# Performance work log

Measured on AMD Instinct MI355X. Metric: run time of the kernel, lower is better.

The kernel has to match this reference:

```python
import jax, jax.numpy as jnp
import numpy as np

BS, NCH, H, NAGGR, R = 8192, 4, 256, 4, 8  # batch, max_output_degree, h_size, n_aggr, rank


def _xavier(k, shape):
    fan_in = int(np.prod(shape[:-1]))
    fan_out = int(shape[-1])
    s = float(np.sqrt(6.0 / (fan_in + fan_out)))
    return jax.random.uniform(k, shape, jnp.float32, -s, s)


def setup_inputs() -> dict:
    key = jax.random.key(0)
    ks = jax.random.split(key, 6)
    return {
        "neighbour_h": jax.random.normal(ks[0], (BS, NCH, H), jnp.float32),
        "U": _xavier(ks[1], (NCH, NAGGR, H, R)),
        "b": _xavier(ks[2], (NCH, NAGGR, 1, R)),
        "U_out": _xavier(ks[3], (NAGGR, R, H)),
        "b_out": _xavier(ks[4], (NAGGR, 1, H)),
        "T": _xavier(ks[5], (NAGGR,) + (R + 1,) * NCH + (R,)),
    }


def reference(neighbour_h, U, b, U_out, b_out, T):
    bs = neighbour_h.shape[0]
    # per-child projection: matmul([bs,nch,1,1,h], [nch,naggr,h,r]) + b, squeezed -> [bs,nch,naggr,r]
    x = jnp.einsum('bch,cahr->bcar', neighbour_h, U) + b[:, :, 0, :]
    ones = jnp.ones((bs, NAGGR, 1), x.dtype)
    # AugmentedTensor chained contraction (vectorized over the n_aggr loop):
    # first mode: [bs,naggr,r+1] @ [naggr,r+1,(r+1)^(nch-1)*r]
    h0 = jnp.concatenate([x[:, 0], ones], axis=-1)          # [bs,naggr,r+1]
    ris = jnp.einsum('baq,aqx->bax', h0, T.reshape(NAGGR, R + 1, -1))
    for i in range(1, NCH):  # contract remaining modes one by one
        hi = jnp.concatenate([x[:, i], ones], axis=-1)      # [bs,naggr,r+1]
        ris = ris.reshape(bs, NAGGR, R + 1, -1)
        ris = jnp.einsum('baq,baqx->bax', hi, ris)
    # ris: [bs,naggr,r]; output projection + bias -> [bs,naggr,h] -> [bs,naggr*h]
    out = jnp.einsum('bar,arh->bah', ris, U_out) + b_out[:, 0, :]
    return out.reshape(bs, -1)
```

## Files before the change

### kernel.cpp

```cpp
#include <hip/hip_runtime.h>

#define TT_ISTRIDE 672
#define TT_ELEMS (4 * 81 * 672)
#define CHUNK_FLOATS (9 * 672)
#define CHUNK_F4 (CHUNK_FLOATS / 4)

__global__ void t_transpose(const float* __restrict__ T, float* __restrict__ Tt) {
    int idx = blockIdx.x * 256 + threadIdx.x;
    if (idx >= TT_ELEMS) return;
    int col  = idx % 84;
    int t1   = idx / 84;
    int r    = t1 & 7;
    int rest = t1 / 8;
    int jt   = col / 28;
    int kk   = col - jt * 28;
    Tt[idx] = (kk < 27) ? T[rest * 648 + (jt * 27 + kk) * 8 + r] : 0.0f;
}

#define GLL(gsrc, ldst) __builtin_amdgcn_global_load_lds( \
    (const __attribute__((address_space(1))) void*)(gsrc), \
    (__attribute__((address_space(3))) void*)(ldst), 16, 0, 0)

__global__ __launch_bounds__(512, 4) void hosvd_fused(
    const float* __restrict__ nh,
    const float* __restrict__ U,
    const float* __restrict__ bi,
    const float* __restrict__ Uo,
    const float* __restrict__ bo,
    const float* __restrict__ Tt,
    float* __restrict__ out) {
    __shared__ union {
        float u[4 * 256 * 8];
        float tc[2][CHUNK_FLOATS];
    } sm;
    __shared__ float uo_lds[8 * 256];
    __shared__ float h_t[36][64];
    __shared__ float ris_s[64][8];

    const int t    = threadIdx.x;
    const int lane = t & 63;
    const int widr = t >> 6;
    const int wg   = (blockIdx.x & 7) * 64 + (blockIdx.x >> 3);
    const int a    = wg & 3;
    const int b0   = (wg >> 2) << 6;

    for (int idx = t; idx < 8192; idx += 512) {
        int c   = idx >> 11;
        int rem = idx & 2047;
        sm.u[idx] = U[((c * 4 + a) << 11) + rem];
    }
    for (int idx = t; idx < 2048; idx += 512)
        uo_lds[idx] = Uo[(a << 11) + idx];
    __syncthreads();

    {
        const int c  = widr >> 1;
        const int r0 = (widr & 1) << 2;
        const float* nhp   = nh + (size_t)(b0 + lane) * 1024 + (size_t)c * 256;
        const float* ubase = sm.u + (c << 11) + r0;
        float4 acc = make_float4(0.f, 0.f, 0.f, 0.f);
        #pragma unroll 4
        for (int h = 0; h < 256; h += 4) {
            float4 v  = *(const float4*)(nhp + h);
            float4 u0 = *(const float4*)(ubase + ((h + 0) << 3));
            float4 u1 = *(const float4*)(ubase + ((h + 1) << 3));
            float4 u2 = *(const float4*)(ubase + ((h + 2) << 3));
            float4 u3 = *(const float4*)(ubase + ((h + 3) << 3));
            acc.x = fmaf(v.x, u0.x, acc.x); acc.y = fmaf(v.x, u0.y, acc.y);
            acc.z = fmaf(v.x, u0.z, acc.z); acc.w = fmaf(v.x, u0.w, acc.w);
            acc.x = fmaf(v.y, u1.x, acc.x); acc.y = fmaf(v.y, u1.y, acc.y);
            acc.z = fmaf(v.y, u1.z, acc.z); acc.w = fmaf(v.y, u1.w, acc.w);
            acc.x = fmaf(v.z, u2.x, acc.x); acc.y = fmaf(v.z, u2.y, acc.y);
            acc.z = fmaf(v.z, u2.z, acc.z); acc.w = fmaf(v.z, u2.w, acc.w);
            acc.x = fmaf(v.w, u3.x, acc.x); acc.y = fmaf(v.w, u3.y, acc.y);
            acc.z = fmaf(v.w, u3.z, acc.z); acc.w = fmaf(v.w, u3.w, acc.w);
        }
        const float4 bb4 = *(const float4*)&bi[((c * 4 + a) << 3) + r0];
        h_t[c * 9 + r0 + 0][lane] = acc.x + bb4.x;
        h_t[c * 9 + r0 + 1][lane] = acc.y + bb4.y;
        h_t[c * 9 + r0 + 2][lane] = acc.z + bb4.z;
        h_t[c * 9 + r0 + 3][lane] = acc.w + bb4.w;
        if (r0) h_t[c * 9 + 8][lane] = 1.0f;
    }
    __syncthreads();

    {
        float h0v[9], h1v[9], h2v[9], h3v[9];
        #pragma unroll
        for (int q = 0; q < 9; ++q) {
            h0v[q] = h_t[q][lane];
            h1v[q] = h_t[9 + q][lane];
            h2v[q] = h_t[18 + q][lane];
            h3v[q] = h_t[27 + q][lane];
        }
        const float* Tw = Tt + (size_t)(a * 81) * TT_ISTRIDE;
        float A = 0.0f;

        {
            const float* s = Tw;
            float* d = sm.tc[0];
            GLL(s + 4 * t, d + 4 * t);
            GLL(s + 4 * (512 + t), d + 4 * (512 + t));
            if (t < CHUNK_F4 - 1024) GLL(s + 4 * (1024 + t), d + 4 * (1024 + t));
        }

        #pragma unroll 1
        for (int c = 0; c < 9; ++c) {
            if (c < 8) {
                const float* s = Tw + (size_t)(c + 1) * CHUNK_FLOATS;
                float* d = sm.tc[(c + 1) & 1];
                GLL(s + 4 * t, d + 4 * t);
                GLL(s + 4 * (512 + t), d + 4 * (512 + t));
                if (t < CHUNK_F4 - 1024) GLL(s + 4 * (1024 + t), d + 4 * (1024 + t));
                asm volatile("s_waitcnt vmcnt(3)" ::: "memory");
            } else {
                asm volatile("s_waitcnt vmcnt(0)" ::: "memory");
            }
            __builtin_amdgcn_s_barrier();
            asm volatile("" ::: "memory");

            const float* tcp = sm.tc[c & 1] + widr * 84;
            const float h0c  = h0v[c];
            #pragma unroll 1
            for (int q1 = 0; q1 < 9; ++q1) {
                const float* tp = tcp + q1 * TT_ISTRIDE;
                float dd = 0.0f;
                #pragma unroll
                for (int jt = 0; jt < 3; ++jt) {
                    float s[28];
                    #pragma unroll
                    for (int m = 0; m < 7; ++m)
                        *(float4*)(s + 4 * m) = *(const float4*)(tp + jt * 28 + 4 * m);
                    float e0 = 0.f, e1 = 0.f, e2 = 0.f;
                    #pragma unroll
                    for (int m = 0; m < 9; ++m) {
                        e0 = fmaf(s[m],      h3v[m], e0);
                        e1 = fmaf(s[9 + m],  h3v[m], e1);
                        e2 = fmaf(s[18 + m], h3v[m], e2);
                    }
                    dd += fmaf(h2v[3 * jt + 2], e2,
                           fmaf(h2v[3 * jt + 1], e1, h2v[3 * jt] * e0));
                }
                A = fmaf(h0c * h1v[q1], dd, A);
            }
            asm volatile("" ::: "memory");
            __builtin_amdgcn_s_barrier();
        }
        ris_s[lane][widr] = A;
    }
    __syncthreads();

    {
        const int h  = t & 255;
        const int bh = t >> 8;
        const float bov = bo[(a << 8) + h];
        const float u0 = uo_lds[h],            u1 = uo_lds[256 + h];
        const float u2 = uo_lds[512 + h],      u3 = uo_lds[768 + h];
        const float u4 = uo_lds[1024 + h],     u5 = uo_lds[1280 + h];
        const float u6 = uo_lds[1536 + h],     u7 = uo_lds[1792 + h];
        float* op = out + (size_t)(b0 + (bh << 5)) * 1024 + (a << 8) + h;
        #pragma unroll 4
        for (int bb = 0; bb < 32; ++bb) {
            const int bidx = (bh << 5) + bb;
            const float4 rlo = *(const float4*)&ris_s[bidx][0];
            const float4 rhi = *(const float4*)&ris_s[bidx][4];
            float v = bov;
            v = fmaf(rlo.x, u0, v); v = fmaf(rlo.y, u1, v);
            v = fmaf(rlo.z, u2, v); v = fmaf(rlo.w, u3, v);
            v = fmaf(rhi.x, u4, v); v = fmaf(rhi.y, u5, v);
            v = fmaf(rhi.z, u6, v); v = fmaf(rhi.w, u7, v);
            op[(size_t)bb * 1024] = v;
        }
    }
}

extern "C" void kernel_launch(void* const* d_in, const int* in_sizes, int n_in,
                              void* d_out, int out_size, void* d_ws, size_t ws_size,
                              hipStream_t stream) {
    (void)in_sizes; (void)n_in; (void)out_size; (void)ws_size;
    const float* nh = (const float*)d_in[0];
    const float* U  = (const float*)d_in[1];
    const float* bi = (const float*)d_in[2];
    const float* Uo = (const float*)d_in[3];
    const float* bo = (const float*)d_in[4];
    const float* T  = (const float*)d_in[5];
    float* outp = (float*)d_out;
    float* Tt   = (float*)d_ws;

    t_transpose<<<(TT_ELEMS + 255) / 256, 256, 0, stream>>>(T, Tt);
    hosvd_fused<<<512, 512, 0, stream>>>(nh, U, bi, Uo, bo, Tt, outp);
}
```

Measured before the change: 100.3 us.

## Process two 64-row batch tiles per workgroup to reuse staged T chunks

Each workgroup now handles 128 batch rows instead of 64, with each thread computing two rows (A and B) in the projection and tensor contraction. Every T chunk loaded into LDS is reused for twice as many rows, so global-to-LDS traffic and barriers per row are halved. The grid drops to 256 blocks and launch bounds relax to 2 blocks per CU. This raises register pressure and lowers parallelism and occupancy, which on a large-CU GPU may leave some CUs idle.

```diff
diff --git a/kernel.cpp b/kernel.cpp
--- a/kernel.cpp
+++ b/kernel.cpp
@@ -21,7 +21,7 @@
     (const __attribute__((address_space(1))) void*)(gsrc), \
     (__attribute__((address_space(3))) void*)(ldst), 16, 0, 0)
 
-__global__ __launch_bounds__(512, 4) void hosvd_fused(
+__global__ __launch_bounds__(512, 2) void hosvd_fused(
     const float* __restrict__ nh,
     const float* __restrict__ U,
     const float* __restrict__ bi,
@@ -34,15 +34,15 @@
         float tc[2][CHUNK_FLOATS];
     } sm;
     __shared__ float uo_lds[8 * 256];
-    __shared__ float h_t[36][64];
-    __shared__ float ris_s[64][8];
+    __shared__ float h_t[36][128];
+    __shared__ float ris_s[128][8];
 
     const int t    = threadIdx.x;
     const int lane = t & 63;
     const int widr = t >> 6;
-    const int wg   = (blockIdx.x & 7) * 64 + (blockIdx.x >> 3);
+    const int wg   = (blockIdx.x & 7) * 32 + (blockIdx.x >> 3);
     const int a    = wg & 3;
-    const int b0   = (wg >> 2) << 6;
+    const int b0   = (wg >> 2) << 7;
 
     for (int idx = t; idx < 8192; idx += 512) {
         int c   = idx >> 11;
@@ -56,45 +56,64 @@
     {
         const int c  = widr >> 1;
         const int r0 = (widr & 1) << 2;
-        const float* nhp   = nh + (size_t)(b0 + lane) * 1024 + (size_t)c * 256;
+        const float* nhA   = nh + (size_t)(b0 + lane) * 1024 + (size_t)c * 256;
+        const float* nhB   = nhA + 64 * 1024;
         const float* ubase = sm.u + (c << 11) + r0;
-        float4 acc = make_float4(0.f, 0.f, 0.f, 0.f);
+        float4 accA = make_float4(0.f, 0.f, 0.f, 0.f);
+        float4 accB = make_float4(0.f, 0.f, 0.f, 0.f);
         #pragma unroll 4
         for (int h = 0; h < 256; h += 4) {
-            float4 v  = *(const float4*)(nhp + h);
+            float4 vA = *(const float4*)(nhA + h);
+            float4 vB = *(const float4*)(nhB + h);
             float4 u0 = *(const float4*)(ubase + ((h + 0) << 3));
             float4 u1 = *(const float4*)(ubase + ((h + 1) << 3));
             float4 u2 = *(const float4*)(ubase + ((h + 2) << 3));
             float4 u3 = *(const float4*)(ubase + ((h + 3) << 3));
-            acc.x = fmaf(v.x, u0.x, acc.x); acc.y = fmaf(v.x, u0.y, acc.y);
-            acc.z = fmaf(v.x, u0.z, acc.z); acc.w = fmaf(v.x, u0.w, acc.w);
-            acc.x = fmaf(v.y, u1.x, acc.x); acc.y = fmaf(v.y, u1.y, acc.y);
-            acc.z = fmaf(v.y, u1.z, acc.z); acc.w = fmaf(v.y, u1.w, acc.w);
-            acc.x = fmaf(v.z, u2.x, acc.x); acc.y = fmaf(v.z, u2.y, acc.y);
-            acc.z = fmaf(v.z, u2.z, acc.z); acc.w = fmaf(v.z, u2.w, acc.w);
-            acc.x = fmaf(v.w, u3.x, acc.x); acc.y = fmaf(v.w, u3.y, acc.y);
-            acc.z = fmaf(v.w, u3.z, acc.z); acc.w = fmaf(v.w, u3.w, acc.w);
+            accA.x = fmaf(vA.x, u0.x, accA.x); accA.y = fmaf(vA.x, u0.y, accA.y);
+            accA.z = fmaf(vA.x, u0.z, accA.z); accA.w = fmaf(vA.x, u0.w, accA.w);
+            accA.x = fmaf(vA.y, u1.x, accA.x); accA.y = fmaf(vA.y, u1.y, accA.y);
+            accA.z = fmaf(vA.y, u1.z, accA.z); accA.w = fmaf(vA.y, u1.w, accA.w);
+            accA.x = fmaf(vA.z, u2.x, accA.x); accA.y = fmaf(vA.z, u2.y, accA.y);
+            accA.z = fmaf(vA.z, u2.z, accA.z); accA.w = fmaf(vA.z, u2.w, accA.w);
+            accA.x = fmaf(vA.w, u3.x, accA.x); accA.y = fmaf(vA.w, u3.y, accA.y);
+            accA.z = fmaf(vA.w, u3.z, accA.z); accA.w = fmaf(vA.w, u3.w, accA.w);
+            accB.x = fmaf(vB.x, u0.x, accB.x); accB.y = fmaf(vB.x, u0.y, accB.y);
+            accB.z = fmaf(vB.x, u0.z, accB.z); accB.w = fmaf(vB.x, u0.w, accB.w);
+            accB.x = fmaf(vB.y, u1.x, accB.x); accB.y = fmaf(vB.y, u1.y, accB.y);
+            accB.z = fmaf(vB.y, u1.z, accB.z); accB.w = fmaf(vB.y, u1.w, accB.w);
+            accB.x = fmaf(vB.z, u2.x, accB.x); accB.y = fmaf(vB.z, u2.y, accB.y);
+            accB.z = fmaf(vB.z, u2.z, accB.z); accB.w = fmaf(vB.z, u2.w, accB.w);
+            accB.x = fmaf(vB.w, u3.x, accB.x); accB.y = fmaf(vB.w, u3.y, accB.y);
+            accB.z = fmaf(vB.w, u3.z, accB.z); accB.w = fmaf(vB.w, u3.w, accB.w);
         }
         const float4 bb4 = *(const float4*)&bi[((c * 4 + a) << 3) + r0];
-        h_t[c * 9 + r0 + 0][lane] = acc.x + bb4.x;
-        h_t[c * 9 + r0 + 1][lane] = acc.y + bb4.y;
-        h_t[c * 9 + r0 + 2][lane] = acc.z + bb4.z;
-        h_t[c * 9 + r0 + 3][lane] = acc.w + bb4.w;
-        if (r0) h_t[c * 9 + 8][lane] = 1.0f;
+        h_t[c * 9 + r0 + 0][lane]      = accA.x + bb4.x;
+        h_t[c * 9 + r0 + 1][lane]      = accA.y + bb4.y;
+        h_t[c * 9 + r0 + 2][lane]      = accA.z + bb4.z;
+        h_t[c * 9 + r0 + 3][lane]      = accA.w + bb4.w;
+        h_t[c * 9 + r0 + 0][lane + 64] = accB.x + bb4.x;
+        h_t[c * 9 + r0 + 1][lane + 64] = accB.y + bb4.y;
+        h_t[c * 9 + r0 + 2][lane + 64] = accB.z + bb4.z;
+        h_t[c * 9 + r0 + 3][lane + 64] = accB.w + bb4.w;
+        if (r0) {
+            h_t[c * 9 + 8][lane]      = 1.0f;
+            h_t[c * 9 + 8][lane + 64] = 1.0f;
+        }
     }
     __syncthreads();
 
     {
-        float h0v[9], h1v[9], h2v[9], h3v[9];
+        float h0A[9], h1A[9], h2A[9], h3A[9];
+        float h0B[9], h1B[9], h2B[9], h3B[9];
         #pragma unroll
         for (int q = 0; q < 9; ++q) {
-            h0v[q] = h_t[q][lane];
-            h1v[q] = h_t[9 + q][lane];
-            h2v[q] = h_t[18 + q][lane];
-            h3v[q] = h_t[27 + q][lane];
+            h0A[q] = h_t[q][lane];      h0B[q] = h_t[q][lane + 64];
+            h1A[q] = h_t[9 + q][lane];  h1B[q] = h_t[9 + q][lane + 64];
+            h2A[q] = h_t[18 + q][lane]; h2B[q] = h_t[18 + q][lane + 64];
+            h3A[q] = h_t[27 + q][lane]; h3B[q] = h_t[27 + q][lane + 64];
         }
         const float* Tw = Tt + (size_t)(a * 81) * TT_ISTRIDE;
-        float A = 0.0f;
+        float AA = 0.0f, AB = 0.0f;
 
         {
             const float* s = Tw;
@@ -120,33 +139,41 @@
             asm volatile("" ::: "memory");
 
             const float* tcp = sm.tc[c & 1] + widr * 84;
-            const float h0c  = h0v[c];
-            #pragma unroll 1
+            const float h0cA = h0A[c], h0cB = h0B[c];
+            #pragma unroll 3
             for (int q1 = 0; q1 < 9; ++q1) {
                 const float* tp = tcp + q1 * TT_ISTRIDE;
-                float dd = 0.0f;
+                float ddA = 0.0f, ddB = 0.0f;
                 #pragma unroll
                 for (int jt = 0; jt < 3; ++jt) {
                     float s[28];
                     #pragma unroll
                     for (int m = 0; m < 7; ++m)
                         *(float4*)(s + 4 * m) = *(const float4*)(tp + jt * 28 + 4 * m);
-                    float e0 = 0.f, e1 = 0.f, e2 = 0.f;
+                    float e0A = 0.f, e1A = 0.f, e2A = 0.f;
+                    float e0B = 0.f, e1B = 0.f, e2B = 0.f;
                     #pragma unroll
                     for (int m = 0; m < 9; ++m) {
-                        e0 = fmaf(s[m],      h3v[m], e0);
-                        e1 = fmaf(s[9 + m],  h3v[m], e1);
-                        e2 = fmaf(s[18 + m], h3v[m], e2);
+                        e0A = fmaf(s[m],      h3A[m], e0A);
+                        e1A = fmaf(s[9 + m],  h3A[m], e1A);
+                        e2A = fmaf(s[18 + m], h3A[m], e2A);
+                        e0B = fmaf(s[m],      h3B[m], e0B);
+                        e1B = fmaf(s[9 + m],  h3B[m], e1B);
+                        e2B = fmaf(s[18 + m], h3B[m], e2B);
                     }
-                    dd += fmaf(h2v[3 * jt + 2], e2,
-                           fmaf(h2v[3 * jt + 1], e1, h2v[3 * jt] * e0));
+                    ddA = fmaf(h2A[3 * jt], e0A, fmaf(h2A[3 * jt + 1], e1A,
+                          fmaf(h2A[3 * jt + 2], e2A, ddA)));
+                    ddB = fmaf(h2B[3 * jt], e0B, fmaf(h2B[3 * jt + 1], e1B,
+                          fmaf(h2B[3 * jt + 2], e2B, ddB)));
                 }
-                A = fmaf(h0c * h1v[q1], dd, A);
+                AA = fmaf(h0cA * h1A[q1], ddA, AA);
+                AB = fmaf(h0cB * h1B[q1], ddB, AB);
             }
             asm volatile("" ::: "memory");
             __builtin_amdgcn_s_barrier();
         }
-        ris_s[lane][widr] = A;
+        ris_s[lane][widr]      = AA;
+        ris_s[lane + 64][widr] = AB;
     }
     __syncthreads();
 
@@ -158,10 +185,10 @@
         const float u2 = uo_lds[512 + h],      u3 = uo_lds[768 + h];
         const float u4 = uo_lds[1024 + h],     u5 = uo_lds[1280 + h];
         const float u6 = uo_lds[1536 + h],     u7 = uo_lds[1792 + h];
-        float* op = out + (size_t)(b0 + (bh << 5)) * 1024 + (a << 8) + h;
+        float* op = out + (size_t)(b0 + (bh << 6)) * 1024 + (a << 8) + h;
         #pragma unroll 4
-        for (int bb = 0; bb < 32; ++bb) {
-            const int bidx = (bh << 5) + bb;
+        for (int bb = 0; bb < 64; ++bb) {
+            const int bidx = (bh << 6) + bb;
             const float4 rlo = *(const float4*)&ris_s[bidx][0];
             const float4 rhi = *(const float4*)&ris_s[bidx][4];
             float v = bov;
@@ -188,5 +215,5 @@
     float* Tt   = (float*)d_ws;
 
     t_transpose<<<(TT_ELEMS + 255) / 256, 256, 0, stream>>>(T, Tt);
-    hosvd_fused<<<512, 512, 0, stream>>>(nh, U, bi, Uo, bo, Tt, outp);
+    hosvd_fused<<<256, 512, 0, stream>>>(nh, U, bi, Uo, bo, Tt, outp);
 }
```

Measured after the change: 96.55 us. 1.04x faster.

## Split fused kernel into projection, chain-contraction and output kernels with 4x batch reuse

Applied to the files above, without the earlier changes.

Replaces the single fused kernel with three kernels. The first computes the per-child projections into a workspace. The second streams the core tensor through LDS for 256 batch rows per block, giving each thread four batch rows so every tensor chunk load is reused four times, and splits the first-mode index across two halves for parallelism. The third sums the two partial results and applies the output projection with vectorized stores. This cuts how often the core tensor is re-read from LDS and global memory, at the cost of extra launches, workspace round-trips and higher register pressure.

```diff
diff --git a/kernel.cpp b/kernel.cpp
--- a/kernel.cpp
+++ b/kernel.cpp
@@ -2,8 +2,9 @@
 
 #define TT_ISTRIDE 672
 #define TT_ELEMS (4 * 81 * 672)
-#define CHUNK_FLOATS (9 * 672)
-#define CHUNK_F4 (CHUNK_FLOATS / 4)
+#define WS_H   217728
+#define WS_RIS 1397376
+#define RIS_IHALF_STRIDE 262144
 
 __global__ void t_transpose(const float* __restrict__ T, float* __restrict__ Tt) {
     int idx = blockIdx.x * 256 + threadIdx.x;
@@ -21,156 +22,207 @@
     (const __attribute__((address_space(1))) void*)(gsrc), \
     (__attribute__((address_space(3))) void*)(ldst), 16, 0, 0)
 
-__global__ __launch_bounds__(512, 4) void hosvd_fused(
-    const float* __restrict__ nh,
-    const float* __restrict__ U,
-    const float* __restrict__ bi,
-    const float* __restrict__ Uo,
-    const float* __restrict__ bo,
-    const float* __restrict__ Tt,
-    float* __restrict__ out) {
-    __shared__ union {
-        float u[4 * 256 * 8];
-        float tc[2][CHUNK_FLOATS];
-    } sm;
-    __shared__ float uo_lds[8 * 256];
-    __shared__ float h_t[36][64];
-    __shared__ float ris_s[64][8];
+#define KEEP(x) asm volatile("" : "+v"(x))
+
+__global__ __launch_bounds__(512, 4) void k1_phasex(
+    const float* __restrict__ nh, const float* __restrict__ U,
+    const float* __restrict__ bi, float* __restrict__ h_ws) {
+    __shared__ float nh_s[128 * 68];
+    __shared__ float u_s[8 * 68];
+    const int t  = threadIdx.x;
+    const int a  = blockIdx.x >> 6;
+    const int b0 = (blockIdx.x & 63) << 7;
+    const int b  = t & 127;
+    const int rp = t >> 7;
+
+    #pragma unroll 1
+    for (int c = 0; c < 4; ++c) {
+        float acc0 = 0.f, acc1 = 0.f;
+        #pragma unroll 1
+        for (int hq = 0; hq < 4; ++hq) {
+            __syncthreads();
+            #pragma unroll
+            for (int k = 0; k < 4; ++k) {
+                int idx = t + (k << 9);
+                int row = idx >> 4, col = (idx & 15) << 2;
+                *(float4*)(nh_s + row * 68 + col) =
+                    *(const float4*)(nh + (size_t)(b0 + row) * 1024 + (c << 8) + (hq << 6) + col);
+            }
+            u_s[(t & 7) * 68 + (t >> 3)] =
+                U[(((c << 2) + a) << 11) + (((hq << 6) + (t >> 3)) << 3) + (t & 7)];
+            __syncthreads();
+            const float* nhp = nh_s + b * 68;
+            const float* u0p = u_s + rp * 68;
+            const float* u1p = u_s + (rp + 4) * 68;
+            #pragma unroll
+            for (int hh = 0; hh < 64; hh += 4) {
+                float4 v  = *(const float4*)(nhp + hh);
+                float4 ua = *(const float4*)(u0p + hh);
+                float4 ub = *(const float4*)(u1p + hh);
+                acc0 = fmaf(v.x, ua.x, acc0); acc0 = fmaf(v.y, ua.y, acc0);
+                acc0 = fmaf(v.z, ua.z, acc0); acc0 = fmaf(v.w, ua.w, acc0);
+                acc1 = fmaf(v.x, ub.x, acc1); acc1 = fmaf(v.y, ub.y, acc1);
+                acc1 = fmaf(v.z, ub.z, acc1); acc1 = fmaf(v.w, ub.w, acc1);
+            }
+        }
+        acc0 += bi[(((c << 2) + a) << 3) + rp];
+        acc1 += bi[(((c << 2) + a) << 3) + rp + 4];
+        size_t hb = ((size_t)a * 8192 + b0 + b) * 36 + c * 9;
+        h_ws[hb + rp]     = acc0;
+        h_ws[hb + rp + 4] = acc1;
+        if (rp == 0) h_ws[hb + 8] = 1.0f;
+    }
+}
+
+__global__ __launch_bounds__(512, 2) void k2_chain(
+    const float* __restrict__ Tt, const float* __restrict__ h_ws,
+    float* __restrict__ risP) {
+    __shared__ float tc[2][9 * 672];
+    __shared__ float h_s[36 * 260];
 
     const int t    = threadIdx.x;
     const int lane = t & 63;
     const int widr = t >> 6;
-    const int wg   = (blockIdx.x & 7) * 64 + (blockIdx.x >> 3);
-    const int a    = wg & 3;
-    const int b0   = (wg >> 2) << 6;
-
-    for (int idx = t; idx < 8192; idx += 512) {
-        int c   = idx >> 11;
-        int rem = idx & 2047;
-        sm.u[idx] = U[((c * 4 + a) << 11) + rem];
-    }
-    for (int idx = t; idx < 2048; idx += 512)
-        uo_lds[idx] = Uo[(a << 11) + idx];
+    const int ihalf = blockIdx.x >> 7;
+    const int a     = (blockIdx.x >> 5) & 3;
+    const int b0    = (blockIdx.x & 31) << 8;
+    const int q0base = ihalf ? 4 : 0;
+    const int NC     = ihalf ? 5 : 4;
+
+    const float* Tw = Tt + (size_t)a * 54432 + (size_t)q0base * 6048;
+
+    {
+        const float* s = Tw;
+        float* d = tc[0];
+        GLL(s + 4 * t, d + 4 * t);
+        GLL(s + 4 * (512 + t), d + 4 * (512 + t));
+        if (t < 488) GLL(s + 4 * (1024 + t), d + 4 * (1024 + t));
+    }
+    for (int idx = t; idx < 2304; idx += 512) {
+        int bb = idx / 9, j = idx % 9;
+        float4 v = *(const float4*)(h_ws + ((size_t)a * 8192 + b0 + bb) * 36 + j * 4);
+        h_s[(4 * j + 0) * 260 + bb] = v.x;
+        h_s[(4 * j + 1) * 260 + bb] = v.y;
+        h_s[(4 * j + 2) * 260 + bb] = v.z;
+        h_s[(4 * j + 3) * 260 + bb] = v.w;
+    }
     __syncthreads();
 
-    {
-        const int c  = widr >> 1;
-        const int r0 = (widr & 1) << 2;
-        const float* nhp   = nh + (size_t)(b0 + lane) * 1024 + (size_t)c * 256;
-        const float* ubase = sm.u + (c << 11) + r0;
-        float4 acc = make_float4(0.f, 0.f, 0.f, 0.f);
-        #pragma unroll 4
-        for (int h = 0; h < 256; h += 4) {
-            float4 v  = *(const float4*)(nhp + h);
-            float4 u0 = *(const float4*)(ubase + ((h + 0) << 3));
-            float4 u1 = *(const float4*)(ubase + ((h + 1) << 3));
-            float4 u2 = *(const float4*)(ubase + ((h + 2) << 3));
-            float4 u3 = *(const float4*)(ubase + ((h + 3) << 3));
-            acc.x = fmaf(v.x, u0.x, acc.x); acc.y = fmaf(v.x, u0.y, acc.y);
-            acc.z = fmaf(v.x, u0.z, acc.z); acc.w = fmaf(v.x, u0.w, acc.w);
-            acc.x = fmaf(v.y, u1.x, acc.x); acc.y = fmaf(v.y, u1.y, acc.y);
-            acc.z = fmaf(v.y, u1.z, acc.z); acc.w = fmaf(v.y, u1.w, acc.w);
-            acc.x = fmaf(v.z, u2.x, acc.x); acc.y = fmaf(v.z, u2.y, acc.y);
-            acc.z = fmaf(v.z, u2.z, acc.z); acc.w = fmaf(v.z, u2.w, acc.w);
-            acc.x = fmaf(v.w, u3.x, acc.x); acc.y = fmaf(v.w, u3.y, acc.y);
-            acc.z = fmaf(v.w, u3.z, acc.z); acc.w = fmaf(v.w, u3.w, acc.w);
-        }
-        const float4 bb4 = *(const float4*)&bi[((c * 4 + a) << 3) + r0];
-        h_t[c * 9 + r0 + 0][lane] = acc.x + bb4.x;
-        h_t[c * 9 + r0 + 1][lane] = acc.y + bb4.y;
-        h_t[c * 9 + r0 + 2][lane] = acc.z + bb4.z;
-        h_t[c * 9 + r0 + 3][lane] = acc.w + bb4.w;
-        if (r0) h_t[c * 9 + 8][lane] = 1.0f;
-    }
-    __syncthreads();
-
-    {
-        float h0v[9], h1v[9], h2v[9], h3v[9];
+    float h2v[4][9], h3v[4][9];
+    #pragma unroll
+    for (int k = 0; k < 4; ++k) {
         #pragma unroll
         for (int q = 0; q < 9; ++q) {
-            h0v[q] = h_t[q][lane];
-            h1v[q] = h_t[9 + q][lane];
-            h2v[q] = h_t[18 + q][lane];
-            h3v[q] = h_t[27 + q][lane];
-        }
-        const float* Tw = Tt + (size_t)(a * 81) * TT_ISTRIDE;
-        float A = 0.0f;
-
-        {
-            const float* s = Tw;
-            float* d = sm.tc[0];
+            h2v[k][q] = h_s[(18 + q) * 260 + lane + 64 * k];
+            h3v[k][q] = h_s[(27 + q) * 260 + lane + 64 * k];
+        }
+    }
+    #pragma unroll
+    for (int k = 0; k < 4; ++k) {
+        #pragma unroll
+        for (int q = 0; q < 9; ++q) { KEEP(h2v[k][q]); KEEP(h3v[k][q]); }
+    }
+
+    float A0 = 0.f, A1 = 0.f, A2 = 0.f, A3 = 0.f;
+
+    #pragma unroll 1
+    for (int c = 0; c < NC; ++c) {
+        if (c < NC - 1) {
+            const float* s = Tw + (size_t)(c + 1) * 6048;
+            float* d = tc[(c + 1) & 1];
             GLL(s + 4 * t, d + 4 * t);
             GLL(s + 4 * (512 + t), d + 4 * (512 + t));
-            if (t < CHUNK_F4 - 1024) GLL(s + 4 * (1024 + t), d + 4 * (1024 + t));
-        }
+            if (t < 488) GLL(s + 4 * (1024 + t), d + 4 * (1024 + t));
+            asm volatile("s_waitcnt vmcnt(3)" ::: "memory");
+        } else {
+            asm volatile("s_waitcnt vmcnt(0)" ::: "memory");
+        }
+        __builtin_amdgcn_s_barrier();
+        asm volatile("" ::: "memory");
+
+        const float* tb = tc[c & 1] + widr * 84;
+        float h0c[4];
+        #pragma unroll
+        for (int k = 0; k < 4; ++k)
+            h0c[k] = h_s[(q0base + c) * 260 + lane + 64 * k];
 
         #pragma unroll 1
-        for (int c = 0; c < 9; ++c) {
-            if (c < 8) {
-                const float* s = Tw + (size_t)(c + 1) * CHUNK_FLOATS;
-                float* d = sm.tc[(c + 1) & 1];
-                GLL(s + 4 * t, d + 4 * t);
-                GLL(s + 4 * (512 + t), d + 4 * (512 + t));
-                if (t < CHUNK_F4 - 1024) GLL(s + 4 * (1024 + t), d + 4 * (1024 + t));
-                asm volatile("s_waitcnt vmcnt(3)" ::: "memory");
-            } else {
-                asm volatile("s_waitcnt vmcnt(0)" ::: "memory");
-            }
-            __builtin_amdgcn_s_barrier();
-            asm volatile("" ::: "memory");
-
-            const float* tcp = sm.tc[c & 1] + widr * 84;
-            const float h0c  = h0v[c];
-            #pragma unroll 1
-            for (int q1 = 0; q1 < 9; ++q1) {
-                const float* tp = tcp + q1 * TT_ISTRIDE;
-                float dd = 0.0f;
+        for (int q1 = 0; q1 < 9; ++q1) {
+            float h1q[4];
+            #pragma unroll
+            for (int k = 0; k < 4; ++k)
+                h1q[k] = h_s[(9 + q1) * 260 + lane + 64 * k];
+            const float* tp = tb + q1 * TT_ISTRIDE;
+            float dd[4] = {0.f, 0.f, 0.f, 0.f};
+            #pragma unroll
+            for (int jt = 0; jt < 3; ++jt) {
+                float s[28];
                 #pragma unroll
-                for (int jt = 0; jt < 3; ++jt) {
-                    float s[28];
-                    #pragma unroll
-                    for (int m = 0; m < 7; ++m)
-                        *(float4*)(s + 4 * m) = *(const float4*)(tp + jt * 28 + 4 * m);
+                for (int m = 0; m < 7; ++m)
+                    *(float4*)(s + 4 * m) = *(const float4*)(tp + jt * 28 + 4 * m);
+                #pragma unroll
+                for (int k = 0; k < 4; ++k) {
                     float e0 = 0.f, e1 = 0.f, e2 = 0.f;
                     #pragma unroll
                     for (int m = 0; m < 9; ++m) {
-                        e0 = fmaf(s[m],      h3v[m], e0);
-                        e1 = fmaf(s[9 + m],  h3v[m], e1);
-                        e2 = fmaf(s[18 + m], h3v[m], e2);
+                        e0 = fmaf(s[m],      h3v[k][m], e0);
+                        e1 = fmaf(s[9 + m],  h3v[k][m], e1);
+                        e2 = fmaf(s[18 + m], h3v[k][m], e2);
                     }
-                    dd += fmaf(h2v[3 * jt + 2], e2,
-                           fmaf(h2v[3 * jt + 1], e1, h2v[3 * jt] * e0));
+                    dd[k] = fmaf(h2v[k][3 * jt], e0, fmaf(h2v[k][3 * jt + 1], e1,
+                            fmaf(h2v[k][3 * jt + 2], e2, dd[k])));
                 }
-                A = fmaf(h0c * h1v[q1], dd, A);
             }
-            asm volatile("" ::: "memory");
-            __builtin_amdgcn_s_barrier();
-        }
-        ris_s[lane][widr] = A;
+            A0 = fmaf(h0c[0] * h1q[0], dd[0], A0);
+            A1 = fmaf(h0c[1] * h1q[1], dd[1], A1);
+            A2 = fmaf(h0c[2] * h1q[2], dd[2], A2);
+            A3 = fmaf(h0c[3] * h1q[3], dd[3], A3);
+        }
+        asm volatile("" ::: "memory");
+        __builtin_amdgcn_s_barrier();
+    }
+
+    size_t rb = (size_t)ihalf * RIS_IHALF_STRIDE + ((size_t)a * 8192 + b0) * 8 + widr;
+    risP[rb + (size_t)(lane)       * 8] = A0;
+    risP[rb + (size_t)(lane + 64)  * 8] = A1;
+    risP[rb + (size_t)(lane + 128) * 8] = A2;
+    risP[rb + (size_t)(lane + 192) * 8] = A3;
+}
+
+__global__ __launch_bounds__(256, 8) void k3_out(
+    const float* __restrict__ risP, const float* __restrict__ Uo,
+    const float* __restrict__ bo, float* __restrict__ out) {
+    __shared__ float uo_s[8192];
+    __shared__ float bo_s[1024];
+    __shared__ float ris_s[16 * 32];
+    const int t  = threadIdx.x;
+    const int b0 = blockIdx.x << 4;
+    for (int idx = t; idx < 8192; idx += 256) uo_s[idx] = Uo[idx];
+    for (int idx = t; idx < 1024; idx += 256) bo_s[idx] = bo[idx];
+    for (int idx = t; idx < 512; idx += 256) {
+        int bb = idx >> 5, rem = idx & 31, aa = rem >> 3, rr = rem & 7;
+        size_t ro = ((size_t)aa * 8192 + b0 + bb) * 8 + rr;
+        ris_s[bb * 32 + rem] = risP[ro] + risP[RIS_IHALF_STRIDE + ro];
     }
     __syncthreads();
-
-    {
-        const int h  = t & 255;
-        const int bh = t >> 8;
-        const float bov = bo[(a << 8) + h];
-        const float u0 = uo_lds[h],            u1 = uo_lds[256 + h];
-        const float u2 = uo_lds[512 + h],      u3 = uo_lds[768 + h];
-        const float u4 = uo_lds[1024 + h],     u5 = uo_lds[1280 + h];
-        const float u6 = uo_lds[1536 + h],     u7 = uo_lds[1792 + h];
-        float* op = out + (size_t)(b0 + (bh << 5)) * 1024 + (a << 8) + h;
-        #pragma unroll 4
-        for (int bb = 0; bb < 32; ++bb) {
-            const int bidx = (bh << 5) + bb;
-            const float4 rlo = *(const float4*)&ris_s[bidx][0];
-            const float4 rhi = *(const float4*)&ris_s[bidx][4];
-            float v = bov;
-            v = fmaf(rlo.x, u0, v); v = fmaf(rlo.y, u1, v);
-            v = fmaf(rlo.z, u2, v); v = fmaf(rlo.w, u3, v);
-            v = fmaf(rhi.x, u4, v); v = fmaf(rhi.y, u5, v);
-            v = fmaf(rhi.z, u6, v); v = fmaf(rhi.w, u7, v);
-            op[(size_t)bb * 1024] = v;
-        }
+    const int a  = t >> 6;
+    const int c4 = (t & 63) << 2;
+    float4 u[8];
+    #pragma unroll
+    for (int r = 0; r < 8; ++r)
+        u[r] = *(const float4*)(uo_s + (a << 11) + (r << 8) + c4);
+    const float4 b4 = *(const float4*)(bo_s + (a << 8) + c4);
+    #pragma unroll 4
+    for (int bb = 0; bb < 16; ++bb) {
+        const float* rp = ris_s + bb * 32 + a * 8;
+        float4 v = b4;
+        #pragma unroll
+        for (int r = 0; r < 8; ++r) {
+            float w = rp[r];
+            v.x = fmaf(w, u[r].x, v.x); v.y = fmaf(w, u[r].y, v.y);
+            v.z = fmaf(w, u[r].z, v.z); v.w = fmaf(w, u[r].w, v.w);
+        }
+        *(float4*)(out + (size_t)(b0 + bb) * 1024 + (a << 8) + c4) = v;
     }
 }
 
@@ -185,8 +237,10 @@
     const float* bo = (const float*)d_in[4];
     const float* T  = (const float*)d_in[5];
     float* outp = (float*)d_out;
-    float* Tt   = (float*)d_ws;
-
-    t_transpose<<<(TT_ELEMS + 255) / 256, 256, 0, stream>>>(T, Tt);
-    hosvd_fused<<<512, 512, 0, stream>>>(nh, U, bi, Uo, bo, Tt, outp);
-}
+    float* ws   = (float*)d_ws;
+
+    t_transpose<<<(TT_ELEMS + 255) / 256, 256, 0, stream>>>(T, ws);
+    k1_phasex<<<256, 512, 0, stream>>>(nh, U, bi, ws + WS_H);
+    k2_chain<<<256, 512, 0, stream>>>(ws, ws + WS_H, ws + WS_RIS);
+    k3_out<<<512, 256, 0, stream>>>(ws + WS_RIS, Uo, bo, outp);
+}
```

New measurement: 108.7 us. 1.08x slower.
